# Optimization experiments

Hardware: AMD Instinct MI355X
Metric: run time of the kernel (lower is better)

The kernel has to match this reference:

```python
import jax, jax.numpy as jnp
import numpy as np

B, T, I, H, O = 64, 512, 128, 1024, 128
ALPHA = 0.2


def setup_inputs() -> dict:
    key = jax.random.key(0)
    ks = jax.random.split(key, 7)
    inv_sqrt_h = 1.0 / np.sqrt(H)
    return {
        "x": jax.random.normal(ks[0], (B, T, I), dtype=jnp.float32),
        "wi": jax.random.normal(ks[1], (I, H), dtype=jnp.float32) / np.sqrt(I),
        "wrec": jax.random.normal(ks[2], (H, H), dtype=jnp.float32) * inv_sqrt_h,
        "wout": jax.random.normal(ks[3], (H, O), dtype=jnp.float32) * inv_sqrt_h,
        "b": jax.random.normal(ks[4], (H, 1), dtype=jnp.float32) * 0.1,
        "g": jax.random.normal(ks[5], (H, 1), dtype=jnp.float32) * 0.5 + 1.0,
        "h0": jax.random.normal(ks[6], (H,), dtype=jnp.float32) * 0.1,
    }


def reference(x, wi, wrec, wout, b, g, h0):
    # Leaky tanh RNN: h_{t+1} = h_t + alpha*(-h_t + (g*r_t) @ wrec^T + x_t @ wi)
    #                 r_t = tanh(h_t + b); out_t = (g*r_t) @ wout
    gv = g[:, 0]  # (H,)
    bv = b[:, 0]  # (H,)
    batch = x.shape[0]

    r0 = jnp.tanh(h0 + bv)                     # (H,)
    out0 = (gv * r0) @ wout                    # (O,) broadcast over batch

    h_init = jnp.broadcast_to(h0, (batch, h0.shape[0]))
    r_init = jnp.broadcast_to(r0, (batch, h0.shape[0]))

    # precompute input projection for all steps used in the loop (steps 0..T-2)
    xs = jnp.swapaxes(x[:, :-1, :], 0, 1)      # (T-1, B, I)

    def step(carry, x_t):
        h, r = carry
        h = h + ALPHA * (-h + (gv * r) @ wrec.T + x_t @ wi)
        r = jnp.tanh(h + bv)
        out = (gv * r) @ wout                  # (B, O)
        return (h, r), out

    _, outs = jax.lax.scan(step, (h_init, r_init), xs)   # (T-1, B, O)
    outs = jnp.swapaxes(outs, 0, 1)                      # (B, T-1, O)
    out0b = jnp.broadcast_to(out0, (batch, 1, wout.shape[1]))
    return jnp.concatenate([out0b, outs], axis=1)        # (B, T, O)
```

## Files before the change

### kernel.cpp

```cpp
#include <hip/hip_runtime.h>

#define H 1024
#define I_DIM 128
#define O_DIM 128
#define T_DIM 512
#define ALPHA 0.2f
#define NWG 64
#define GSZ 16

typedef short short8 __attribute__((ext_vector_type(8)));
typedef float f32x4 __attribute__((ext_vector_type(4)));
typedef unsigned long long ull_alias __attribute__((may_alias));

__device__ __forceinline__ unsigned short f2b(float f) {
    union { float f; unsigned u; } x; x.f = f;
    unsigned u = x.u;
    return (unsigned short)((u + 0x7FFFu + ((u >> 16) & 1u)) >> 16);
}
__device__ __forceinline__ float tanh_fast(float x) {
    float e = __expf(2.0f * x);
    return 1.0f - 2.0f * __builtin_amdgcn_rcpf(e + 1.0f);
}
__device__ __forceinline__ short8 ld8f(const float* __restrict__ p) {
    const float4 a = *(const float4*)p;
    const float4 b = *(const float4*)(p + 4);
    short8 r;
    r[0]=(short)f2b(a.x); r[1]=(short)f2b(a.y); r[2]=(short)f2b(a.z); r[3]=(short)f2b(a.w);
    r[4]=(short)f2b(b.x); r[5]=(short)f2b(b.y); r[6]=(short)f2b(b.z); r[7]=(short)f2b(b.w);
    return r;
}

__global__ __launch_bounds__(256, 1) void rnn_kernel(
    const float* __restrict__ x, const float* __restrict__ wi,
    const float* __restrict__ wrec, const float* __restrict__ wout,
    const float* __restrict__ bb, const float* __restrict__ gg,
    const float* __restrict__ h0p, float* __restrict__ out,
    unsigned short* __restrict__ aG, unsigned int* __restrict__ tagG)
{
    __shared__ unsigned short abuf[32 * 512];
    __shared__ unsigned short aloc[1024];
    __shared__ float opart[4 * 128];

    const int tid  = threadIdx.x;
    const int w    = tid >> 6, lane = tid & 63;
    const int n    = lane & 15, q = lane >> 4;
    const int grp  = blockIdx.x & 3;
    const int ji   = blockIdx.x >> 2;
    const int j0   = ji * 64;
    const int j    = j0 + w * 16 + n;
    const int b0   = grp * 16;
    unsigned int* tg = tagG + grp * 128;

    short8 wfr[32];
#pragma unroll
    for (int kt = 0; kt < 32; ++kt)
        wfr[kt] = ld8f(&wrec[(size_t)j * H + kt * 32 + q * 8]);

    short8 wifr[4];
#pragma unroll
    for (int kt = 0; kt < 4; ++kt) {
        short8 v;
#pragma unroll
        for (int i = 0; i < 8; ++i)
            v[i] = (short)f2b(wi[(size_t)(kt * 32 + q * 8 + i) * H + j]);
        wifr[kt] = v;
    }
    short8 wofr[8];
#pragma unroll
    for (int kk = 0; kk < 8; ++kk) {
        short8 v;
        const int kb = (w * 8 + kk) * 32 + q * 8;
#pragma unroll
        for (int i = 0; i < 8; ++i)
            v[i] = (n < 8) ? (short)f2b(wout[(size_t)(kb + i) * O_DIM + ji * 8 + n]) : (short)0;
        wofr[kk] = v;
    }

    const float gv = gg[j], bv = bb[j], h00 = h0p[j];
    float hreg[4];
#pragma unroll
    for (int r = 0; r < 4; ++r) hreg[r] = h00;

    const int kl    = w * 16 + n;
    const int off_l = (kl >> 5) * 512 + ((kl & 31) >> 3) * 128 + (kl & 7);
    const int slot  = ji * 4 + w;

    auto publish = [&](int t) {
        asm volatile("" ::: "memory");
        unsigned long long v = *(const ull_alias*)&aloc[w * 256 + lane * 4];
        unsigned long long* dst = (unsigned long long*)
            (aG + (size_t)((t & 1) * 4 + grp) * 16384 + ji * 1024 + w * 256 + lane * 4);
        __hip_atomic_store(dst, v, __ATOMIC_RELAXED, __HIP_MEMORY_SCOPE_AGENT);
        asm volatile("s_waitcnt vmcnt(0)" ::: "memory");
        if (lane == 0)
            __hip_atomic_store(&tg[(t & 1) * 64 + slot], (unsigned)t,
                               __ATOMIC_RELAXED, __HIP_MEMORY_SCOPE_AGENT);
    };

    auto consume = [&](int tv) {
        const ull_alias* s64 = (const ull_alias*)
            (aG + (size_t)((tv & 1) * 4 + grp) * 16384) + (size_t)w * 1024;
        unsigned long long vals[16];
#pragma unroll
        for (int i = 0; i < 16; ++i)
            vals[i] = __hip_atomic_load((const unsigned long long*)&s64[i * 64 + lane],
                                        __ATOMIC_RELAXED, __HIP_MEMORY_SCOPE_AGENT);
        asm volatile("" ::: "memory");
        ull_alias* d64 = (ull_alias*)abuf + (size_t)w * 1024;
#pragma unroll
        for (int i = 0; i < 16; ++i)
            d64[i * 64 + lane] = vals[i];
    };

    auto do_out = [&](int t) {
        f32x4 oa = {0.f, 0.f, 0.f, 0.f};
#pragma unroll
        for (int kk = 0; kk < 8; ++kk) {
            short8 af = *(const short8*)&abuf[(w * 8 + kk) * 512 + lane * 8];
            oa = __builtin_amdgcn_mfma_f32_16x16x32_bf16(af, wofr[kk], oa, 0, 0, 0);
        }
        if (n < 8) {
#pragma unroll
            for (int r = 0; r < 4; ++r) opart[w * 128 + (4 * q + r) * 8 + n] = oa[r];
        }
        __syncthreads();
        if (tid < 128) {
            float s = opart[tid] + opart[128 + tid] + opart[256 + tid] + opart[384 + tid];
            const int m = tid >> 3, c = tid & 7;
            out[((size_t)(b0 + m) * T_DIM + t) * O_DIM + ji * 8 + c] = s;
        }
    };

    auto wait_tags = [&](int tv) {
        const unsigned int* tp = tg + (tv & 1) * 64;
        for (;;) {
            unsigned v = __hip_atomic_load(&tp[lane], __ATOMIC_RELAXED,
                                           __HIP_MEMORY_SCOPE_AGENT);
            if (__all(v == (unsigned)tv)) break;
            __builtin_amdgcn_s_sleep(1);
        }
        asm volatile("" ::: "memory");
    };

    {
        unsigned short a0 = f2b(gv * tanh_fast(h00 + bv));
#pragma unroll
        for (int r = 0; r < 4; ++r) aloc[off_l + (4 * q + r) * 8] = a0;
        publish(0);
    }

    short8 xfr[4];
#pragma unroll
    for (int kt = 0; kt < 4; ++kt)
        xfr[kt] = ld8f(&x[(size_t)(b0 + n) * T_DIM * I_DIM + kt * 32 + q * 8]);

    for (int t = 1; t < T_DIM; ++t) {
        f32x4 acc0 = {0.f,0.f,0.f,0.f}, acc1 = {0.f,0.f,0.f,0.f};
        acc0 = __builtin_amdgcn_mfma_f32_16x16x32_bf16(xfr[0], wifr[0], acc0, 0,0,0);
        acc1 = __builtin_amdgcn_mfma_f32_16x16x32_bf16(xfr[1], wifr[1], acc1, 0,0,0);
        acc0 = __builtin_amdgcn_mfma_f32_16x16x32_bf16(xfr[2], wifr[2], acc0, 0,0,0);
        acc1 = __builtin_amdgcn_mfma_f32_16x16x32_bf16(xfr[3], wifr[3], acc1, 0,0,0);

        __syncthreads();
        wait_tags(t - 1);
        consume(t - 1);
        __syncthreads();

#pragma unroll
        for (int kt = 0; kt < 32; kt += 2) {
            short8 a0f = *(const short8*)&abuf[kt * 512 + lane * 8];
            short8 a1f = *(const short8*)&abuf[(kt + 1) * 512 + lane * 8];
            acc0 = __builtin_amdgcn_mfma_f32_16x16x32_bf16(a0f, wfr[kt],     acc0, 0,0,0);
            acc1 = __builtin_amdgcn_mfma_f32_16x16x32_bf16(a1f, wfr[kt + 1], acc1, 0,0,0);
        }

#pragma unroll
        for (int r = 0; r < 4; ++r) {
            float z  = acc0[r] + acc1[r];
            float hv = (1.0f - ALPHA) * hreg[r] + ALPHA * z;
            hreg[r] = hv;
            aloc[off_l + (4 * q + r) * 8] = f2b(gv * tanh_fast(hv + bv));
        }
        publish(t);

        if (t < T_DIM - 1) {
#pragma unroll
            for (int kt = 0; kt < 4; ++kt)
                xfr[kt] = ld8f(&x[((size_t)(b0 + n) * T_DIM + t) * I_DIM + kt * 32 + q * 8]);
        }
        do_out(t - 1);
    }

    __syncthreads();
    wait_tags(T_DIM - 1);
    consume(T_DIM - 1);
    __syncthreads();
    do_out(T_DIM - 1);
}

extern "C" void kernel_launch(void* const* d_in, const int* in_sizes, int n_in,
                              void* d_out, int out_size, void* d_ws, size_t ws_size,
                              hipStream_t stream) {
    const float* x    = (const float*)d_in[0];
    const float* wi   = (const float*)d_in[1];
    const float* wrec = (const float*)d_in[2];
    const float* wout = (const float*)d_in[3];
    const float* bb   = (const float*)d_in[4];
    const float* gg   = (const float*)d_in[5];
    const float* h0   = (const float*)d_in[6];
    float* outp = (float*)d_out;

    unsigned short* aG = (unsigned short*)d_ws;
    unsigned int* tagG = (unsigned int*)((char*)d_ws + 2 * 4 * 16384 * 2);

    hipMemsetAsync(tagG, 0xFF, 4 * 2 * 64 * sizeof(unsigned int), stream);
    hipLaunchKernelGGL(rnn_kernel, dim3(NWG), dim3(256), 0, stream,
                       x, wi, wrec, wout, bb, gg, h0, outp, aG, tagG);
}
```

Before: 1.977 ms.

## Embed step tags in published data words to drop separate flag handshake

Each published 64-bit activation chunk is split across two 64-bit stores whose top 16 bits carry the step tag. Consumers spin directly on the data loads until every tag matches. This replaces the store, vmcnt wait, flag store and flag-poll sequence, and drops the memset of the flag array. The cost is twice the bytes per exchange. The workspace is no longer initialised, so correctness relies on stale tags never matching the expected step.

```diff
diff --git a/kernel.cpp b/kernel.cpp
--- a/kernel.cpp
+++ b/kernel.cpp
@@ -35,7 +35,7 @@
     const float* __restrict__ wrec, const float* __restrict__ wout,
     const float* __restrict__ bb, const float* __restrict__ gg,
     const float* __restrict__ h0p, float* __restrict__ out,
-    unsigned short* __restrict__ aG, unsigned int* __restrict__ tagG)
+    unsigned long long* __restrict__ aG)
 {
     __shared__ unsigned short abuf[32 * 512];
     __shared__ unsigned short aloc[1024];
@@ -49,7 +49,6 @@
     const int j0   = ji * 64;
     const int j    = j0 + w * 16 + n;
     const int b0   = grp * 16;
-    unsigned int* tg = tagG + grp * 128;
 
     short8 wfr[32];
 #pragma unroll
@@ -83,33 +82,57 @@
 
     const int kl    = w * 16 + n;
     const int off_l = (kl >> 5) * 512 + ((kl & 31) >> 3) * 128 + (kl & 7);
-    const int slot  = ji * 4 + w;
+    const int upub  = ji * 256 + w * 64 + lane;
 
     auto publish = [&](int t) {
         asm volatile("" ::: "memory");
         unsigned long long v = *(const ull_alias*)&aloc[w * 256 + lane * 4];
-        unsigned long long* dst = (unsigned long long*)
-            (aG + (size_t)((t & 1) * 4 + grp) * 16384 + ji * 1024 + w * 256 + lane * 4);
-        __hip_atomic_store(dst, v, __ATOMIC_RELAXED, __HIP_MEMORY_SCOPE_AGENT);
-        asm volatile("s_waitcnt vmcnt(0)" ::: "memory");
-        if (lane == 0)
-            __hip_atomic_store(&tg[(t & 1) * 64 + slot], (unsigned)t,
-                               __ATOMIC_RELAXED, __HIP_MEMORY_SCOPE_AGENT);
+        const unsigned long long tg = (unsigned long long)(t & 0xFFFF) << 48;
+        unsigned long long s0 = (v & 0x0000FFFFFFFFFFFFull) | tg;
+        unsigned long long s1 = ((v >> 48) & 0xFFFFull) | tg;
+        unsigned long long* dst =
+            aG + (size_t)((t & 1) * 4 + grp) * 8192 + (size_t)upub * 2;
+        __hip_atomic_store(dst + 0, s0, __ATOMIC_RELAXED, __HIP_MEMORY_SCOPE_AGENT);
+        __hip_atomic_store(dst + 1, s1, __ATOMIC_RELAXED, __HIP_MEMORY_SCOPE_AGENT);
     };
 
     auto consume = [&](int tv) {
-        const ull_alias* s64 = (const ull_alias*)
-            (aG + (size_t)((tv & 1) * 4 + grp) * 16384) + (size_t)w * 1024;
-        unsigned long long vals[16];
-#pragma unroll
-        for (int i = 0; i < 16; ++i)
-            vals[i] = __hip_atomic_load((const unsigned long long*)&s64[i * 64 + lane],
-                                        __ATOMIC_RELAXED, __HIP_MEMORY_SCOPE_AGENT);
-        asm volatile("" ::: "memory");
-        ull_alias* d64 = (ull_alias*)abuf + (size_t)w * 1024;
-#pragma unroll
-        for (int i = 0; i < 16; ++i)
-            d64[i * 64 + lane] = vals[i];
+        const unsigned long long want = (unsigned long long)(tv & 0xFFFF);
+        const unsigned long long* src = aG + (size_t)((tv & 1) * 4 + grp) * 8192;
+        ull_alias* d64 = (ull_alias*)abuf;
+#pragma unroll
+        for (int c = 0; c < 4; ++c) {
+            unsigned long long s0[4], s1[4];
+#pragma unroll
+            for (int i = 0; i < 4; ++i) {
+                const unsigned long long* p =
+                    src + (size_t)(w * 1024 + (c * 4 + i) * 64 + lane) * 2;
+                s0[i] = __hip_atomic_load(p + 0, __ATOMIC_RELAXED, __HIP_MEMORY_SCOPE_AGENT);
+                s1[i] = __hip_atomic_load(p + 1, __ATOMIC_RELAXED, __HIP_MEMORY_SCOPE_AGENT);
+            }
+            for (;;) {
+                unsigned bad = 0;
+#pragma unroll
+                for (int i = 0; i < 4; ++i)
+                    if (((s0[i] >> 48) != want) || ((s1[i] >> 48) != want)) bad |= 1u << i;
+                if (__all(bad == 0)) break;
+#pragma unroll
+                for (int i = 0; i < 4; ++i)
+                    if (bad & (1u << i)) {
+                        const unsigned long long* p =
+                            src + (size_t)(w * 1024 + (c * 4 + i) * 64 + lane) * 2;
+                        s0[i] = __hip_atomic_load(p + 0, __ATOMIC_RELAXED, __HIP_MEMORY_SCOPE_AGENT);
+                        s1[i] = __hip_atomic_load(p + 1, __ATOMIC_RELAXED, __HIP_MEMORY_SCOPE_AGENT);
+                    }
+            }
+            asm volatile("" ::: "memory");
+#pragma unroll
+            for (int i = 0; i < 4; ++i) {
+                unsigned long long v = (s0[i] & 0x0000FFFFFFFFFFFFull) |
+                                       ((s1[i] & 0xFFFFull) << 48);
+                d64[(size_t)w * 1024 + (c * 4 + i) * 64 + lane] = v;
+            }
+        }
     };
 
     auto do_out = [&](int t) {
@@ -129,17 +152,6 @@
             const int m = tid >> 3, c = tid & 7;
             out[((size_t)(b0 + m) * T_DIM + t) * O_DIM + ji * 8 + c] = s;
         }
-    };
-
-    auto wait_tags = [&](int tv) {
-        const unsigned int* tp = tg + (tv & 1) * 64;
-        for (;;) {
-            unsigned v = __hip_atomic_load(&tp[lane], __ATOMIC_RELAXED,
-                                           __HIP_MEMORY_SCOPE_AGENT);
-            if (__all(v == (unsigned)tv)) break;
-            __builtin_amdgcn_s_sleep(1);
-        }
-        asm volatile("" ::: "memory");
     };
 
     {
@@ -162,7 +174,6 @@
         acc1 = __builtin_amdgcn_mfma_f32_16x16x32_bf16(xfr[3], wifr[3], acc1, 0,0,0);
 
         __syncthreads();
-        wait_tags(t - 1);
         consume(t - 1);
         __syncthreads();
 
@@ -192,7 +203,6 @@
     }
 
     __syncthreads();
-    wait_tags(T_DIM - 1);
     consume(T_DIM - 1);
     __syncthreads();
     do_out(T_DIM - 1);
@@ -210,10 +220,8 @@
     const float* h0   = (const float*)d_in[6];
     float* outp = (float*)d_out;
 
-    unsigned short* aG = (unsigned short*)d_ws;
-    unsigned int* tagG = (unsigned int*)((char*)d_ws + 2 * 4 * 16384 * 2);
-
-    hipMemsetAsync(tagG, 0xFF, 4 * 2 * 64 * sizeof(unsigned int), stream);
+    unsigned long long* aG = (unsigned long long*)d_ws;
+
     hipLaunchKernelGGL(rnn_kernel, dim3(NWG), dim3(256), 0, stream,
-                       x, wi, wrec, wout, bb, gg, h0, outp, aG, tagG);
-}
+                       x, wi, wrec, wout, bb, gg, h0, outp, aG);
+}
```

Result: slower. 2.343 ms (+18.5%).

## Use 32 workgroups of 512 threads and prefetch tag loads for RNN sync

Applied to the files above, without the earlier changes.

Halves the workgroup count to 32 with 8 waves each, so every workgroup owns 128 hidden units and 16 output columns. This reduces the number of participants in the cross-workgroup spin barrier per step and removes the wasted half of the output MFMA lanes. The tag poll is now issued right after publishing, so its latency overlaps the output computation. In exchange each CU carries twice the register-resident weights across more waves, and the published buffers are laid out as 64-bit words.

```diff
diff --git a/kernel.cpp b/kernel.cpp
--- a/kernel.cpp
+++ b/kernel.cpp
@@ -5,8 +5,8 @@
 #define O_DIM 128
 #define T_DIM 512
 #define ALPHA 0.2f
-#define NWG 64
-#define GSZ 16
+#define NWG 32
+#define GSZ 8
 
 typedef short short8 __attribute__((ext_vector_type(8)));
 typedef float f32x4 __attribute__((ext_vector_type(4)));
@@ -30,23 +30,23 @@
     return r;
 }
 
-__global__ __launch_bounds__(256, 1) void rnn_kernel(
+__global__ __launch_bounds__(512, 2) void rnn_kernel(
     const float* __restrict__ x, const float* __restrict__ wi,
     const float* __restrict__ wrec, const float* __restrict__ wout,
     const float* __restrict__ bb, const float* __restrict__ gg,
     const float* __restrict__ h0p, float* __restrict__ out,
-    unsigned short* __restrict__ aG, unsigned int* __restrict__ tagG)
+    unsigned long long* __restrict__ aG, unsigned int* __restrict__ tagG)
 {
     __shared__ unsigned short abuf[32 * 512];
-    __shared__ unsigned short aloc[1024];
-    __shared__ float opart[4 * 128];
+    __shared__ unsigned short aloc[2048];
+    __shared__ float opart[8 * 256];
 
     const int tid  = threadIdx.x;
     const int w    = tid >> 6, lane = tid & 63;
     const int n    = lane & 15, q = lane >> 4;
     const int grp  = blockIdx.x & 3;
     const int ji   = blockIdx.x >> 2;
-    const int j0   = ji * 64;
+    const int j0   = ji * 128;
     const int j    = j0 + w * 16 + n;
     const int b0   = grp * 16;
     unsigned int* tg = tagG + grp * 128;
@@ -65,14 +65,14 @@
             v[i] = (short)f2b(wi[(size_t)(kt * 32 + q * 8 + i) * H + j]);
         wifr[kt] = v;
     }
-    short8 wofr[8];
-#pragma unroll
-    for (int kk = 0; kk < 8; ++kk) {
+    short8 wofr[4];
+#pragma unroll
+    for (int kk = 0; kk < 4; ++kk) {
         short8 v;
-        const int kb = (w * 8 + kk) * 32 + q * 8;
+        const int kb = w * 128 + kk * 32 + q * 8;
 #pragma unroll
         for (int i = 0; i < 8; ++i)
-            v[i] = (n < 8) ? (short)f2b(wout[(size_t)(kb + i) * O_DIM + ji * 8 + n]) : (short)0;
+            v[i] = (short)f2b(wout[(size_t)(kb + i) * O_DIM + ji * 16 + n]);
         wofr[kk] = v;
     }
 
@@ -83,13 +83,13 @@
 
     const int kl    = w * 16 + n;
     const int off_l = (kl >> 5) * 512 + ((kl & 31) >> 3) * 128 + (kl & 7);
-    const int slot  = ji * 4 + w;
+    const int slot  = ji * 8 + w;
 
     auto publish = [&](int t) {
         asm volatile("" ::: "memory");
         unsigned long long v = *(const ull_alias*)&aloc[w * 256 + lane * 4];
-        unsigned long long* dst = (unsigned long long*)
-            (aG + (size_t)((t & 1) * 4 + grp) * 16384 + ji * 1024 + w * 256 + lane * 4);
+        unsigned long long* dst =
+            aG + (size_t)((t & 1) * 4 + grp) * 4096 + (size_t)(ji * 512 + w * 64 + lane);
         __hip_atomic_store(dst, v, __ATOMIC_RELAXED, __HIP_MEMORY_SCOPE_AGENT);
         asm volatile("s_waitcnt vmcnt(0)" ::: "memory");
         if (lane == 0)
@@ -97,49 +97,49 @@
                                __ATOMIC_RELAXED, __HIP_MEMORY_SCOPE_AGENT);
     };
 
+    auto load_tags = [&](int tv) -> unsigned {
+        return __hip_atomic_load(&tg[(tv & 1) * 64 + lane], __ATOMIC_RELAXED,
+                                 __HIP_MEMORY_SCOPE_AGENT);
+    };
+
     auto consume = [&](int tv) {
-        const ull_alias* s64 = (const ull_alias*)
-            (aG + (size_t)((tv & 1) * 4 + grp) * 16384) + (size_t)w * 1024;
-        unsigned long long vals[16];
-#pragma unroll
-        for (int i = 0; i < 16; ++i)
-            vals[i] = __hip_atomic_load((const unsigned long long*)&s64[i * 64 + lane],
-                                        __ATOMIC_RELAXED, __HIP_MEMORY_SCOPE_AGENT);
+        const unsigned long long* src = aG + (size_t)((tv & 1) * 4 + grp) * 4096;
+        unsigned long long s0[4], s1[4];
+#pragma unroll
+        for (int i = 0; i < 4; ++i) {
+            const int c = 4 * w + i;
+            s0[i] = __hip_atomic_load(src + (size_t)c * 128 + lane,
+                                      __ATOMIC_RELAXED, __HIP_MEMORY_SCOPE_AGENT);
+            s1[i] = __hip_atomic_load(src + (size_t)c * 128 + 64 + lane,
+                                      __ATOMIC_RELAXED, __HIP_MEMORY_SCOPE_AGENT);
+        }
         asm volatile("" ::: "memory");
-        ull_alias* d64 = (ull_alias*)abuf + (size_t)w * 1024;
-#pragma unroll
-        for (int i = 0; i < 16; ++i)
-            d64[i * 64 + lane] = vals[i];
+        ull_alias* d64 = (ull_alias*)abuf;
+#pragma unroll
+        for (int i = 0; i < 4; ++i) {
+            const int c = 4 * w + i;
+            d64[(size_t)c * 128 + lane]      = s0[i];
+            d64[(size_t)c * 128 + 64 + lane] = s1[i];
+        }
     };
 
     auto do_out = [&](int t) {
         f32x4 oa = {0.f, 0.f, 0.f, 0.f};
 #pragma unroll
-        for (int kk = 0; kk < 8; ++kk) {
-            short8 af = *(const short8*)&abuf[(w * 8 + kk) * 512 + lane * 8];
+        for (int kk = 0; kk < 4; ++kk) {
+            short8 af = *(const short8*)&abuf[(4 * w + kk) * 512 + lane * 8];
             oa = __builtin_amdgcn_mfma_f32_16x16x32_bf16(af, wofr[kk], oa, 0, 0, 0);
         }
-        if (n < 8) {
-#pragma unroll
-            for (int r = 0; r < 4; ++r) opart[w * 128 + (4 * q + r) * 8 + n] = oa[r];
-        }
+#pragma unroll
+        for (int r = 0; r < 4; ++r) opart[w * 256 + (4 * q + r) * 16 + n] = oa[r];
         __syncthreads();
-        if (tid < 128) {
-            float s = opart[tid] + opart[128 + tid] + opart[256 + tid] + opart[384 + tid];
-            const int m = tid >> 3, c = tid & 7;
-            out[((size_t)(b0 + m) * T_DIM + t) * O_DIM + ji * 8 + c] = s;
-        }
-    };
-
-    auto wait_tags = [&](int tv) {
-        const unsigned int* tp = tg + (tv & 1) * 64;
-        for (;;) {
-            unsigned v = __hip_atomic_load(&tp[lane], __ATOMIC_RELAXED,
-                                           __HIP_MEMORY_SCOPE_AGENT);
-            if (__all(v == (unsigned)tv)) break;
-            __builtin_amdgcn_s_sleep(1);
-        }
-        asm volatile("" ::: "memory");
+        if (tid < 256) {
+            float s = 0.f;
+#pragma unroll
+            for (int wv = 0; wv < 8; ++wv) s += opart[wv * 256 + tid];
+            const int m = tid >> 4, c = tid & 15;
+            out[((size_t)(b0 + m) * T_DIM + t) * O_DIM + ji * 16 + c] = s;
+        }
     };
 
     {
@@ -148,6 +148,7 @@
         for (int r = 0; r < 4; ++r) aloc[off_l + (4 * q + r) * 8] = a0;
         publish(0);
     }
+    unsigned tagv = load_tags(0);
 
     short8 xfr[4];
 #pragma unroll
@@ -162,7 +163,11 @@
         acc1 = __builtin_amdgcn_mfma_f32_16x16x32_bf16(xfr[3], wifr[3], acc1, 0,0,0);
 
         __syncthreads();
-        wait_tags(t - 1);
+        while (!__all(tagv == (unsigned)(t - 1))) {
+            __builtin_amdgcn_s_sleep(1);
+            tagv = load_tags(t - 1);
+        }
+        asm volatile("" ::: "memory");
         consume(t - 1);
         __syncthreads();
 
@@ -182,6 +187,7 @@
             aloc[off_l + (4 * q + r) * 8] = f2b(gv * tanh_fast(hv + bv));
         }
         publish(t);
+        tagv = load_tags(t);
 
         if (t < T_DIM - 1) {
 #pragma unroll
@@ -192,7 +198,11 @@
     }
 
     __syncthreads();
-    wait_tags(T_DIM - 1);
+    while (!__all(tagv == (unsigned)(T_DIM - 1))) {
+        __builtin_amdgcn_s_sleep(1);
+        tagv = load_tags(T_DIM - 1);
+    }
+    asm volatile("" ::: "memory");
     consume(T_DIM - 1);
     __syncthreads();
     do_out(T_DIM - 1);
@@ -210,10 +220,10 @@
     const float* h0   = (const float*)d_in[6];
     float* outp = (float*)d_out;
 
-    unsigned short* aG = (unsigned short*)d_ws;
-    unsigned int* tagG = (unsigned int*)((char*)d_ws + 2 * 4 * 16384 * 2);
+    unsigned long long* aG = (unsigned long long*)d_ws;
+    unsigned int* tagG = (unsigned int*)((char*)d_ws + 262144);
 
     hipMemsetAsync(tagG, 0xFF, 4 * 2 * 64 * sizeof(unsigned int), stream);
-    hipLaunchKernelGGL(rnn_kernel, dim3(NWG), dim3(256), 0, stream,
+    hipLaunchKernelGGL(rnn_kernel, dim3(NWG), dim3(512), 0, stream,
                        x, wi, wrec, wout, bb, gg, h0, outp, aG, tagG);
 }
```

Measured after the change: 3.313 ms. 67.6% more time.
